# Performance work log

Measured on AMD Instinct MI355X. Metric: run time of the kernel, lower is better.

The kernel has to match this reference:

```python
import jax, jax.numpy as jnp
import numpy as np

D_MODEL = 1024
NUM_HEADS = 16
HEAD_DIM = D_MODEL // NUM_HEADS


def setup_inputs() -> dict:
    key = jax.random.key(0)
    k_x, k_wqkv, k_bqkv, k_wfc, k_bfc = jax.random.split(key, 5)
    scale_in = 1.0 / np.sqrt(D_MODEL)
    return {
        "x": jax.random.normal(k_x, (2, 2048, D_MODEL), dtype=jnp.float32),
        # torch nn.Linear stores weight as [out_features, in_features]
        "w_qkv": jax.random.uniform(k_wqkv, (3 * D_MODEL, D_MODEL), jnp.float32, -scale_in, scale_in),
        "b_qkv": jax.random.uniform(k_bqkv, (3 * D_MODEL,), jnp.float32, -scale_in, scale_in),
        "w_fc": jax.random.uniform(k_wfc, (D_MODEL, D_MODEL), jnp.float32, -scale_in, scale_in),
        "b_fc": jax.random.uniform(k_bfc, (D_MODEL,), jnp.float32, -scale_in, scale_in),
    }


def reference(x, w_qkv, b_qkv, w_fc, b_fc):
    B, S, _ = x.shape
    # fused QKV projection: [B,S,3*d_model]
    qkv = jnp.einsum("bsd,ed->bse", x, w_qkv) + b_qkv
    # [B,S,H,3*head_dim] -> [B,H,S,3*head_dim]
    qkv = qkv.reshape(B, S, NUM_HEADS, 3 * HEAD_DIM).transpose(0, 2, 1, 3)
    Q, K, V = jnp.split(qkv, 3, axis=-1)  # each [B,H,S,head_dim]
    scores = jnp.einsum("bhqd,bhkd->bhqk", Q, K) / np.sqrt(HEAD_DIM).astype(np.float32)
    attention = jax.nn.softmax(scores, axis=-1)  # [B,H,S,S]
    values = jnp.einsum("bhqk,bhkd->bhqd", attention, V)
    # [B,H,S,head_dim] -> [B,S,d_model]
    values = values.transpose(0, 2, 1, 3).reshape(B, S, D_MODEL)
    out = jnp.einsum("bsd,ed->bse", values, w_fc) + b_fc
    return out
```

## Files before the change

### kernel.cpp

```cpp
#include <hip/hip_runtime.h>
#include <hip/hip_bf16.h>

#define D_MODEL 1024
#define NH 16
#define HD 64
#define BATCH 2
#define SEQ 2048

typedef __attribute__((ext_vector_type(8))) short short8;
typedef __attribute__((ext_vector_type(4))) float floatx4;

static __device__ __forceinline__ short f2bf(float f) {
    __hip_bfloat16 h = __float2bfloat16(f);
    return *reinterpret_cast<short*>(&h);
}

__global__ __launch_bounds__(256) void cvt_f32_bf16(
    const float* __restrict__ src, short* __restrict__ dst)
{
    int i = blockIdx.x * 256 + threadIdx.x;
    float4 a = *reinterpret_cast<const float4*>(src + i * 8);
    float4 b = *reinterpret_cast<const float4*>(src + i * 8 + 4);
    short8 o;
    o[0] = f2bf(a.x); o[1] = f2bf(a.y); o[2] = f2bf(a.z); o[3] = f2bf(a.w);
    o[4] = f2bf(b.x); o[5] = f2bf(b.y); o[6] = f2bf(b.z); o[7] = f2bf(b.w);
    *reinterpret_cast<short8*>(dst + i * 8) = o;
}

__global__ __launch_bounds__(256) void qkv_gemm(
    const short* __restrict__ X, const short* __restrict__ W,
    const float* __restrict__ bias,
    short* __restrict__ Qs, short* __restrict__ Ks, short* __restrict__ Vt_g)
{
    __shared__ __align__(16) short As[128][72];
    __shared__ __align__(16) short Bs[128][72];
    const int tid = threadIdx.x;
    const int m0 = blockIdx.y * 128;
    const int n0 = blockIdx.x * 128;
    const int w = tid >> 6, lane = tid & 63;
    const int quad = lane >> 4, l15 = lane & 15;
    const int wm = (w >> 1) * 64, wn = (w & 1) * 64;

    floatx4 acc[4][4];
#pragma unroll
    for (int i = 0; i < 4; i++)
#pragma unroll
        for (int j = 0; j < 4; j++) acc[i][j] = (floatx4)0.0f;

    for (int k0 = 0; k0 < 1024; k0 += 64) {
        __syncthreads();
#pragma unroll
        for (int i = 0; i < 4; i++) {
            int c = tid + i * 256;
            int row = c >> 3, ck = c & 7;
            *reinterpret_cast<uint4*>(&As[row][ck * 8]) =
                *reinterpret_cast<const uint4*>(&X[(m0 + row) * 1024 + k0 + ck * 8]);
            *reinterpret_cast<uint4*>(&Bs[row][ck * 8]) =
                *reinterpret_cast<const uint4*>(&W[(n0 + row) * 1024 + k0 + ck * 8]);
        }
        __syncthreads();
#pragma unroll
        for (int kk = 0; kk < 2; kk++) {
            short8 a[4], b[4];
#pragma unroll
            for (int t = 0; t < 4; t++) {
                a[t] = *reinterpret_cast<const short8*>(&As[wm + t * 16 + l15][kk * 32 + quad * 8]);
                b[t] = *reinterpret_cast<const short8*>(&Bs[wn + t * 16 + l15][kk * 32 + quad * 8]);
            }
#pragma unroll
            for (int mt = 0; mt < 4; mt++)
#pragma unroll
                for (int nt = 0; nt < 4; nt++)
                    acc[mt][nt] = __builtin_amdgcn_mfma_f32_16x16x32_bf16(
                        a[mt], b[nt], acc[mt][nt], 0, 0, 0);
        }
    }

#pragma unroll
    for (int nt = 0; nt < 4; nt++) {
        int col = n0 + wn + nt * 16 + l15;
        float bv = bias[col];
        int h = col / 192;
        int j = col - h * 192;
#pragma unroll
        for (int mt = 0; mt < 4; mt++) {
#pragma unroll
            for (int r = 0; r < 4; r++) {
                int row = m0 + wm + mt * 16 + quad * 4 + r;
                float v = acc[mt][nt][r] + bv;
                int bi = row >> 11, s = row & 2047;
                int bh = bi * NH + h;
                if (j < 64)       Qs[(bh * SEQ + s) * HD + j] = f2bf(v * 0.125f);
                else if (j < 128) Ks[(bh * SEQ + s) * HD + (j - 64)] = f2bf(v);
                else              Vt_g[(bh * HD + (j - 128)) * SEQ + s] = f2bf(v);
            }
        }
    }
}

__global__ __launch_bounds__(256) void attn_kernel(
    const short* __restrict__ Qs, const short* __restrict__ Ks,
    const short* __restrict__ Vt_g, short* __restrict__ attn)
{
    __shared__ __align__(16) short Kl[64][72];
    __shared__ __align__(16) short Vt[64][72];
    __shared__ __align__(16) short Pl[4][16][72];

    const int tid = threadIdx.x;
    const int w = tid >> 6, lane = tid & 63;
    const int quad = lane >> 4, l15 = lane & 15;
    const int q0 = blockIdx.x * 64;
    const int h = blockIdx.y, bi = blockIdx.z;
    const int bh = bi * NH + h;
    const int kbase = bh * SEQ * HD;
    const int vbase = bh * HD * SEQ;

    short8 aq[2];
    {
        int qrow = q0 + w * 16 + l15;
        const short* qp = Qs + kbase + qrow * HD;
        aq[0] = *reinterpret_cast<const short8*>(qp + quad * 8);
        aq[1] = *reinterpret_cast<const short8*>(qp + 32 + quad * 8);
    }

    float l_r[4] = {0.f, 0.f, 0.f, 0.f};
    floatx4 o[4];
#pragma unroll
    for (int nt = 0; nt < 4; nt++) o[nt] = (floatx4)0.0f;

    for (int kt = 0; kt < SEQ; kt += 64) {
        __syncthreads();
#pragma unroll
        for (int i = 0; i < 2; i++) {
            int c = tid + i * 256;
            int row = c >> 3, ck = c & 7;
            *reinterpret_cast<uint4*>(&Kl[row][ck * 8]) =
                *reinterpret_cast<const uint4*>(&Ks[kbase + (kt + row) * HD + ck * 8]);
            *reinterpret_cast<uint4*>(&Vt[row][ck * 8]) =
                *reinterpret_cast<const uint4*>(&Vt_g[vbase + row * SEQ + kt + ck * 8]);
        }
        __syncthreads();

        floatx4 sf[4];
#pragma unroll
        for (int nt = 0; nt < 4; nt++) sf[nt] = (floatx4)0.0f;
#pragma unroll
        for (int c = 0; c < 2; c++) {
#pragma unroll
            for (int nt = 0; nt < 4; nt++) {
                short8 bk = *reinterpret_cast<const short8*>(&Kl[nt * 16 + l15][c * 32 + quad * 8]);
                sf[nt] = __builtin_amdgcn_mfma_f32_16x16x32_bf16(aq[c], bk, sf[nt], 0, 0, 0);
            }
        }

#pragma unroll
        for (int nt = 0; nt < 4; nt++) {
#pragma unroll
            for (int r = 0; r < 4; r++) {
                float e = __expf(sf[nt][r]);
                l_r[r] += e;
                Pl[w][quad * 4 + r][nt * 16 + l15] = f2bf(e);
            }
        }
        asm volatile("s_waitcnt lgkmcnt(0)" ::: "memory");

#pragma unroll
        for (int c = 0; c < 2; c++) {
            short8 ap = *reinterpret_cast<const short8*>(&Pl[w][l15][c * 32 + quad * 8]);
#pragma unroll
            for (int nt = 0; nt < 4; nt++) {
                short8 bv = *reinterpret_cast<const short8*>(&Vt[nt * 16 + l15][c * 32 + quad * 8]);
                o[nt] = __builtin_amdgcn_mfma_f32_16x16x32_bf16(ap, bv, o[nt], 0, 0, 0);
            }
        }
    }

#pragma unroll
    for (int r = 0; r < 4; r++) {
#pragma unroll
        for (int mask = 1; mask < 16; mask <<= 1)
            l_r[r] += __shfl_xor(l_r[r], mask);
    }

#pragma unroll
    for (int nt = 0; nt < 4; nt++) {
#pragma unroll
        for (int r = 0; r < 4; r++) {
            int row = q0 + w * 16 + quad * 4 + r;
            int col = h * HD + nt * 16 + l15;
            attn[(bi * SEQ + row) * D_MODEL + col] = f2bf(o[nt][r] / l_r[r]);
        }
    }
}

__global__ __launch_bounds__(256) void fc_gemm(
    const short* __restrict__ A, const short* __restrict__ W,
    const float* __restrict__ bias, float* __restrict__ out)
{
    __shared__ __align__(16) short As[128][72];
    __shared__ __align__(16) short Bs[128][72];
    const int tid = threadIdx.x;
    const int m0 = blockIdx.y * 128;
    const int n0 = blockIdx.x * 128;
    const int w = tid >> 6, lane = tid & 63;
    const int quad = lane >> 4, l15 = lane & 15;
    const int wm = (w >> 1) * 64, wn = (w & 1) * 64;

    floatx4 acc[4][4];
#pragma unroll
    for (int i = 0; i < 4; i++)
#pragma unroll
        for (int j = 0; j < 4; j++) acc[i][j] = (floatx4)0.0f;

    for (int k0 = 0; k0 < 1024; k0 += 64) {
        __syncthreads();
#pragma unroll
        for (int i = 0; i < 4; i++) {
            int c = tid + i * 256;
            int row = c >> 3, ck = c & 7;
            *reinterpret_cast<uint4*>(&As[row][ck * 8]) =
                *reinterpret_cast<const uint4*>(&A[(m0 + row) * 1024 + k0 + ck * 8]);
            *reinterpret_cast<uint4*>(&Bs[row][ck * 8]) =
                *reinterpret_cast<const uint4*>(&W[(n0 + row) * 1024 + k0 + ck * 8]);
        }
        __syncthreads();
#pragma unroll
        for (int kk = 0; kk < 2; kk++) {
            short8 a[4], b[4];
#pragma unroll
            for (int t = 0; t < 4; t++) {
                a[t] = *reinterpret_cast<const short8*>(&As[wm + t * 16 + l15][kk * 32 + quad * 8]);
                b[t] = *reinterpret_cast<const short8*>(&Bs[wn + t * 16 + l15][kk * 32 + quad * 8]);
            }
#pragma unroll
            for (int mt = 0; mt < 4; mt++)
#pragma unroll
                for (int nt = 0; nt < 4; nt++)
                    acc[mt][nt] = __builtin_amdgcn_mfma_f32_16x16x32_bf16(
                        a[mt], b[nt], acc[mt][nt], 0, 0, 0);
        }
    }

#pragma unroll
    for (int nt = 0; nt < 4; nt++) {
        int col = n0 + wn + nt * 16 + l15;
        float bv = bias[col];
#pragma unroll
        for (int mt = 0; mt < 4; mt++) {
#pragma unroll
            for (int r = 0; r < 4; r++) {
                int row = m0 + wm + mt * 16 + quad * 4 + r;
                out[row * 1024 + col] = acc[mt][nt][r] + bv;
            }
        }
    }
}

extern "C" void kernel_launch(void* const* d_in, const int* in_sizes, int n_in,
                              void* d_out, int out_size, void* d_ws, size_t ws_size,
                              hipStream_t stream) {
    const float* x     = (const float*)d_in[0];
    const float* w_qkv = (const float*)d_in[1];
    const float* b_qkv = (const float*)d_in[2];
    const float* w_fc  = (const float*)d_in[3];
    const float* b_fc  = (const float*)d_in[4];
    float* out = (float*)d_out;

    const size_t M4 = 4u * 1024 * 1024;
    short* Xb    = (short*)d_ws;
    short* Wqb   = Xb + M4;
    short* Wfb   = Wqb + 3u * 1024 * 1024;
    short* Qs    = Wfb + 1024 * 1024;
    short* Ks    = Qs + M4;
    short* Vt_g  = Ks + M4;
    short* attnb = Xb;

    cvt_f32_bf16<<<2048, 256, 0, stream>>>(x, Xb);
    cvt_f32_bf16<<<1536, 256, 0, stream>>>(w_qkv, Wqb);
    cvt_f32_bf16<<<512,  256, 0, stream>>>(w_fc, Wfb);

    qkv_gemm<<<dim3(24, 32), 256, 0, stream>>>(Xb, Wqb, b_qkv, Qs, Ks, Vt_g);
    attn_kernel<<<dim3(32, 16, 2), 256, 0, stream>>>(Qs, Ks, Vt_g, attnb);
    fc_gemm<<<dim3(8, 32), 256, 0, stream>>>(attnb, Wfb, b_fc, out);
}
```

Measured before the change: 228.9 us.

## Split attention key tile across warp pairs and merge conversion launches

The attention kernel now gives each warp 32 query rows and half of each 64-key tile instead of 16 query rows and the full tile. Each loaded K fragment then feeds two MFMAs, and the two warp halves combine their partial outputs and row sums through shared memory at the end. The three fp32-to-bf16 conversion kernels are merged into one launch. This cuts per-tile LDS reads of K and V and saves two kernel launches, at the cost of an extra shared-memory reduction and more accumulator registers.

After: 227.8 us. Within noise of the previous version (-0.5%).

```diff
diff --git a/kernel.cpp b/kernel.cpp
--- a/kernel.cpp
+++ b/kernel.cpp
@@ -15,16 +15,22 @@
     return *reinterpret_cast<short*>(&h);
 }
 
-__global__ __launch_bounds__(256) void cvt_f32_bf16(
-    const float* __restrict__ src, short* __restrict__ dst)
+__global__ __launch_bounds__(256) void cvt_all(
+    const float* __restrict__ x, const float* __restrict__ wq,
+    const float* __restrict__ wf,
+    short* __restrict__ Xb, short* __restrict__ Wqb, short* __restrict__ Wfb)
 {
     int i = blockIdx.x * 256 + threadIdx.x;
-    float4 a = *reinterpret_cast<const float4*>(src + i * 8);
-    float4 b = *reinterpret_cast<const float4*>(src + i * 8 + 4);
+    const float* src; short* dst; int off;
+    if (i < 524288)      { src = x;  dst = Xb;  off = i; }
+    else if (i < 917504) { src = wq; dst = Wqb; off = i - 524288; }
+    else                 { src = wf; dst = Wfb; off = i - 917504; }
+    float4 a = *reinterpret_cast<const float4*>(src + off * 8);
+    float4 b = *reinterpret_cast<const float4*>(src + off * 8 + 4);
     short8 o;
     o[0] = f2bf(a.x); o[1] = f2bf(a.y); o[2] = f2bf(a.z); o[3] = f2bf(a.w);
     o[4] = f2bf(b.x); o[5] = f2bf(b.y); o[6] = f2bf(b.z); o[7] = f2bf(b.w);
-    *reinterpret_cast<short8*>(dst + i * 8) = o;
+    *reinterpret_cast<short8*>(dst + off * 8) = o;
 }
 
 __global__ __launch_bounds__(256) void qkv_gemm(
@@ -102,12 +108,17 @@
     const short* __restrict__ Qs, const short* __restrict__ Ks,
     const short* __restrict__ Vt_g, short* __restrict__ attn)
 {
-    __shared__ __align__(16) short Kl[64][72];
-    __shared__ __align__(16) short Vt[64][72];
-    __shared__ __align__(16) short Pl[4][16][72];
+    __shared__ __align__(16) char smem[2 * 64 * 72 * 2];
+    __shared__ __align__(16) short Pl[4][32][40];
+    __shared__ float Ls[64];
+
+    short (*Kl)[72] = (short(*)[72])smem;
+    short (*Vt)[72] = (short(*)[72])(smem + 64 * 72 * 2);
+    float (*Osum)[66] = (float(*)[66])smem;
 
     const int tid = threadIdx.x;
     const int w = tid >> 6, lane = tid & 63;
+    const int wq = w >> 1, wk = w & 1;
     const int quad = lane >> 4, l15 = lane & 15;
     const int q0 = blockIdx.x * 64;
     const int h = blockIdx.y, bi = blockIdx.z;
@@ -115,18 +126,24 @@
     const int kbase = bh * SEQ * HD;
     const int vbase = bh * HD * SEQ;
 
-    short8 aq[2];
-    {
-        int qrow = q0 + w * 16 + l15;
-        const short* qp = Qs + kbase + qrow * HD;
-        aq[0] = *reinterpret_cast<const short8*>(qp + quad * 8);
-        aq[1] = *reinterpret_cast<const short8*>(qp + 32 + quad * 8);
-    }
-
-    float l_r[4] = {0.f, 0.f, 0.f, 0.f};
-    floatx4 o[4];
-#pragma unroll
-    for (int nt = 0; nt < 4; nt++) o[nt] = (floatx4)0.0f;
+    short8 aq[2][2];
+#pragma unroll
+    for (int mt = 0; mt < 2; mt++) {
+        const short* qp = Qs + kbase + (q0 + wq * 32 + mt * 16 + l15) * HD;
+#pragma unroll
+        for (int c = 0; c < 2; c++)
+            aq[mt][c] = *reinterpret_cast<const short8*>(qp + c * 32 + quad * 8);
+    }
+
+    float l_acc[2][4];
+    floatx4 o[2][4];
+#pragma unroll
+    for (int mt = 0; mt < 2; mt++) {
+#pragma unroll
+        for (int r = 0; r < 4; r++) l_acc[mt][r] = 0.f;
+#pragma unroll
+        for (int nt = 0; nt < 4; nt++) o[mt][nt] = (floatx4)0.0f;
+    }
 
     for (int kt = 0; kt < SEQ; kt += 64) {
         __syncthreads();
@@ -141,54 +158,88 @@
         }
         __syncthreads();
 
-        floatx4 sf[4];
-#pragma unroll
-        for (int nt = 0; nt < 4; nt++) sf[nt] = (floatx4)0.0f;
+        floatx4 sf[2][2];
+#pragma unroll
+        for (int mt = 0; mt < 2; mt++)
+#pragma unroll
+            for (int nt = 0; nt < 2; nt++) sf[mt][nt] = (floatx4)0.0f;
 #pragma unroll
         for (int c = 0; c < 2; c++) {
 #pragma unroll
+            for (int nt = 0; nt < 2; nt++) {
+                short8 bk = *reinterpret_cast<const short8*>(
+                    &Kl[wk * 32 + nt * 16 + l15][c * 32 + quad * 8]);
+#pragma unroll
+                for (int mt = 0; mt < 2; mt++)
+                    sf[mt][nt] = __builtin_amdgcn_mfma_f32_16x16x32_bf16(
+                        aq[mt][c], bk, sf[mt][nt], 0, 0, 0);
+            }
+        }
+
+#pragma unroll
+        for (int mt = 0; mt < 2; mt++) {
+#pragma unroll
+            for (int nt = 0; nt < 2; nt++) {
+#pragma unroll
+                for (int r = 0; r < 4; r++) {
+                    float e = __expf(sf[mt][nt][r]);
+                    l_acc[mt][r] += e;
+                    Pl[w][mt * 16 + quad * 4 + r][nt * 16 + l15] = f2bf(e);
+                }
+            }
+        }
+        asm volatile("s_waitcnt lgkmcnt(0)" ::: "memory");
+
+#pragma unroll
+        for (int mt = 0; mt < 2; mt++) {
+            short8 ap = *reinterpret_cast<const short8*>(&Pl[w][mt * 16 + l15][quad * 8]);
+#pragma unroll
             for (int nt = 0; nt < 4; nt++) {
-                short8 bk = *reinterpret_cast<const short8*>(&Kl[nt * 16 + l15][c * 32 + quad * 8]);
-                sf[nt] = __builtin_amdgcn_mfma_f32_16x16x32_bf16(aq[c], bk, sf[nt], 0, 0, 0);
-            }
-        }
-
-#pragma unroll
-        for (int nt = 0; nt < 4; nt++) {
+                short8 bv = *reinterpret_cast<const short8*>(
+                    &Vt[nt * 16 + l15][wk * 32 + quad * 8]);
+                o[mt][nt] = __builtin_amdgcn_mfma_f32_16x16x32_bf16(
+                    ap, bv, o[mt][nt], 0, 0, 0);
+            }
+        }
+    }
+
+#pragma unroll
+    for (int mt = 0; mt < 2; mt++)
+#pragma unroll
+        for (int r = 0; r < 4; r++)
+#pragma unroll
+            for (int mask = 1; mask < 16; mask <<= 1)
+                l_acc[mt][r] += __shfl_xor(l_acc[mt][r], mask);
+
+    __syncthreads();
+    if (wk == 0) {
+#pragma unroll
+        for (int mt = 0; mt < 2; mt++) {
+#pragma unroll
+            for (int nt = 0; nt < 4; nt++)
+#pragma unroll
+                for (int r = 0; r < 4; r++)
+                    Osum[wq * 32 + mt * 16 + quad * 4 + r][nt * 16 + l15] = o[mt][nt][r];
+            if (l15 == 0)
+#pragma unroll
+                for (int r = 0; r < 4; r++)
+                    Ls[wq * 32 + mt * 16 + quad * 4 + r] = l_acc[mt][r];
+        }
+    }
+    __syncthreads();
+    if (wk == 1) {
+#pragma unroll
+        for (int mt = 0; mt < 2; mt++) {
 #pragma unroll
             for (int r = 0; r < 4; r++) {
-                float e = __expf(sf[nt][r]);
-                l_r[r] += e;
-                Pl[w][quad * 4 + r][nt * 16 + l15] = f2bf(e);
-            }
-        }
-        asm volatile("s_waitcnt lgkmcnt(0)" ::: "memory");
-
-#pragma unroll
-        for (int c = 0; c < 2; c++) {
-            short8 ap = *reinterpret_cast<const short8*>(&Pl[w][l15][c * 32 + quad * 8]);
-#pragma unroll
-            for (int nt = 0; nt < 4; nt++) {
-                short8 bv = *reinterpret_cast<const short8*>(&Vt[nt * 16 + l15][c * 32 + quad * 8]);
-                o[nt] = __builtin_amdgcn_mfma_f32_16x16x32_bf16(ap, bv, o[nt], 0, 0, 0);
-            }
-        }
-    }
-
-#pragma unroll
-    for (int r = 0; r < 4; r++) {
-#pragma unroll
-        for (int mask = 1; mask < 16; mask <<= 1)
-            l_r[r] += __shfl_xor(l_r[r], mask);
-    }
-
-#pragma unroll
-    for (int nt = 0; nt < 4; nt++) {
-#pragma unroll
-        for (int r = 0; r < 4; r++) {
-            int row = q0 + w * 16 + quad * 4 + r;
-            int col = h * HD + nt * 16 + l15;
-            attn[(bi * SEQ + row) * D_MODEL + col] = f2bf(o[nt][r] / l_r[r]);
+                int qrow = wq * 32 + mt * 16 + quad * 4 + r;
+                float lt = Ls[qrow] + l_acc[mt][r];
+#pragma unroll
+                for (int nt = 0; nt < 4; nt++) {
+                    float val = (o[mt][nt][r] + Osum[qrow][nt * 16 + l15]) / lt;
+                    attn[(bi * SEQ + q0 + qrow) * D_MODEL + h * HD + nt * 16 + l15] = f2bf(val);
+                }
+            }
         }
     }
 }
@@ -275,10 +326,7 @@
     short* Vt_g  = Ks + M4;
     short* attnb = Xb;
 
-    cvt_f32_bf16<<<2048, 256, 0, stream>>>(x, Xb);
-    cvt_f32_bf16<<<1536, 256, 0, stream>>>(w_qkv, Wqb);
-    cvt_f32_bf16<<<512,  256, 0, stream>>>(w_fc, Wfb);
-
+    cvt_all<<<4096, 256, 0, stream>>>(x, w_qkv, w_fc, Xb, Wqb, Wfb);
     qkv_gemm<<<dim3(24, 32), 256, 0, stream>>>(Xb, Wqb, b_qkv, Qs, Ks, Vt_g);
     attn_kernel<<<dim3(32, 16, 2), 256, 0, stream>>>(Qs, Ks, Vt_g, attnb);
     fc_gemm<<<dim3(8, 32), 256, 0, stream>>>(attnb, Wfb, b_fc, out);
```
